# Performance work log

Measured on AMD Instinct MI355X. Metric: run time of the kernel, lower is better.

Reference implementation:

```python
import jax, jax.numpy as jnp
import numpy as np

OUT = 7  # output_size of AdaptiveMaxPool2d


def _roi_pool(images, rois, roi_idx):
    # images: [N,C,H,W]; rois: [R,4] rel coords (x1,y1,x2,y2); roi_idx: [R]
    n, c, h, w = images.shape
    x1 = jnp.floor(rois[:, 0] * w).astype(jnp.int32)
    y1 = jnp.floor(rois[:, 1] * h).astype(jnp.int32)
    x2 = jnp.ceil(rois[:, 2] * w).astype(jnp.int32)
    y2 = jnp.ceil(rois[:, 3] * h).astype(jnp.int32)
    Hr = y2 - y1  # per-ROI crop height
    Wr = x2 - x1  # per-ROI crop width

    feats = images[roi_idx]  # [R,C,H,W] gather per-ROI source image
    hh = jnp.arange(h)
    ww = jnp.arange(w)
    neg = jnp.finfo(images.dtype).min

    # Adaptive max pool is separable: max over row-bins, then col-bins.
    # PyTorch adaptive bins over a region of size L: [floor(i*L/OUT), ceil((i+1)*L/OUT))
    rows = []
    for i in range(OUT):  # small fixed loop over output rows
        s = y1 + (i * Hr) // OUT
        e = y1 + ((i + 1) * Hr + OUT - 1) // OUT  # ceil
        m = (hh[None, :] >= s[:, None]) & (hh[None, :] < e[:, None])  # [R,H]
        rows.append(jnp.max(jnp.where(m[:, None, :, None], feats, neg), axis=2))  # [R,C,W]
    rowp = jnp.stack(rows, axis=2)  # [R,C,OUT,W]

    cols = []
    for j in range(OUT):  # small fixed loop over output cols
        s = x1 + (j * Wr) // OUT
        e = x1 + ((j + 1) * Wr + OUT - 1) // OUT
        m = (ww[None, :] >= s[:, None]) & (ww[None, :] < e[:, None])  # [R,W]
        cols.append(jnp.max(jnp.where(m[:, None, None, :], rowp, neg), axis=3))  # [R,C,OUT]
    return jnp.stack(cols, axis=3)  # [R,C,OUT,OUT]


def setup_inputs() -> dict:
    key = jax.random.key(0)
    k1, k2, k3 = jax.random.split(key, 3)
    N, C, H, W, R = 8, 256, 56, 56, 256
    images = jax.random.normal(k1, (N, C, H, W), dtype=jnp.float32)
    # build valid boxes: x1<x2, y1<y2 in [0,1]
    pts = jax.random.uniform(k2, (R, 2, 2), dtype=jnp.float32)
    lo = jnp.min(pts, axis=1)
    hi = jnp.max(pts, axis=1)
    rois = jnp.stack([lo[:, 0], lo[:, 1], hi[:, 0], hi[:, 1]], axis=1)  # [R,4]
    roi_idx = jax.random.randint(k3, (R,), 0, N)
    return {"images": images, "rois": rois, "roi_idx": roi_idx}


def reference(images, rois, roi_idx):
    return _roi_pool(images, rois, roi_idx)
```

## Files before the change

### kernel.cpp

```cpp
#include <hip/hip_runtime.h>

#define OUTS 7
#define CC 256
#define HH 56
#define WW 56
#define PX (HH * WW)
#define STRIDE 58
#define SPLIT 2
#define MAXROI 96

typedef _Float16 half2_t __attribute__((ext_vector_type(2)));

__global__ __launch_bounds__(256) void roipool_kernel(
    const float* __restrict__ images, const float* __restrict__ rois,
    const int* __restrict__ roi_idx, float* __restrict__ out, int R)
{
    __shared__ __align__(16) uint2 plane[STRIDE * HH];
    __shared__ int    list[MAXROI];
    __shared__ unsigned short ys[MAXROI * 7];
    __shared__ unsigned short xs[MAXROI * 7];
    __shared__ int cnt;

    const int b  = blockIdx.x;
    const int s  = b & (SPLIT - 1);
    const int pq = b >> 1;
    const int n  = pq >> 6;
    const int c0 = (pq & 63) * 4;
    const int t  = threadIdx.x;

    if (t < 64) {
        int base = 0;
        #pragma unroll
        for (int k = 0; k < 4; ++k) {
            int r = k * 64 + t;
            bool match = (r < R) && (roi_idx[r] == n);
            unsigned long long mask = __ballot(match);
            int pos = base + __popcll(mask & ((1ULL << t) - 1ULL));
            if (match && pos < MAXROI) list[pos] = r;
            base += __popcll(mask);
        }
        if (t == 0) cnt = (base < MAXROI) ? base : MAXROI;
    }

    const float4* srcA = reinterpret_cast<const float4*>(images + (size_t)(n * CC + c0)     * PX);
    const float4* srcB = reinterpret_cast<const float4*>(images + (size_t)(n * CC + c0 + 1) * PX);
    const float4* srcC = reinterpret_cast<const float4*>(images + (size_t)(n * CC + c0 + 2) * PX);
    const float4* srcD = reinterpret_cast<const float4*>(images + (size_t)(n * CC + c0 + 3) * PX);
    #pragma unroll
    for (int k = 0; k < 4; ++k) {
        int idx = t + k * 256;
        if (idx < PX / 4) {
            float4 a = srcA[idx], bb = srcB[idx], cc = srcC[idx], dd = srcD[idx];
            const float* ap = &a.x; const float* bp = &bb.x;
            const float* cp = &cc.x; const float* dp = &dd.x;
            int y  = idx / 14;
            int x0 = (idx - y * 14) * 4;
            unsigned lo[4], hi[4];
            #pragma unroll
            for (int p = 0; p < 4; ++p) {
                half2_t l = { (_Float16)ap[p], (_Float16)bp[p] };
                half2_t h = { (_Float16)cp[p], (_Float16)dp[p] };
                lo[p] = __builtin_bit_cast(unsigned, l);
                hi[p] = __builtin_bit_cast(unsigned, h);
            }
            uint4* dst = reinterpret_cast<uint4*>(&plane[y * STRIDE + x0]);
            dst[0] = make_uint4(lo[0], hi[0], lo[1], hi[1]);
            dst[1] = make_uint4(lo[2], hi[2], lo[3], hi[3]);
        }
    }
    __syncthreads();

    const int count = cnt;

    for (int e = t; e < count * 7; e += 256) {
        int m = e / 7, i = e - m * 7;
        int r = list[m];
        float4 rv = reinterpret_cast<const float4*>(rois)[r];
        int x1 = (int)floorf(rv.x * (float)WW);
        int y1 = (int)floorf(rv.y * (float)HH);
        int x2 = (int)ceilf (rv.z * (float)WW);
        int y2 = (int)ceilf (rv.w * (float)HH);
        int Hr = y2 - y1, Wr = x2 - x1;
        int sy = y1 + (i * Hr) / 7, ey = y1 + ((i + 1) * Hr + 6) / 7;
        int sx = x1 + (i * Wr) / 7, ex = x1 + ((i + 1) * Wr + 6) / 7;
        ys[m * 7 + i] = (unsigned short)(sy | (ey << 8));
        xs[m * 7 + i] = (unsigned short)(sx | (ex << 8));
    }
    __syncthreads();

    const int wv   = t >> 6;
    const int lane = t & 63;
    const int i = lane / 7;
    const int j = lane - i * 7;

    if (lane < OUTS * OUTS) {
        const half2_t NEG = { (_Float16)-65504.0f, (_Float16)-65504.0f };
        for (int m = (wv << 1) + s; m < count; m += SPLIT * 4) {
            int r = list[m];
            int yse = ys[m * 7 + i];
            int xse = xs[m * 7 + j];
            int sy = yse & 255, ey = yse >> 8;
            int sx = xse & 255, ex = xse >> 8;

            half2_t a01 = NEG, a23 = NEG;

            for (int y = sy; y < ey; y += 2) {
                const uint2* r0 = plane + y * STRIDE;
                const uint2* r1 = plane + min(y + 1, ey - 1) * STRIDE;
                for (int x = sx; x < ex; x += 4) {
                    int xb = min(x + 1, ex - 1);
                    int xc = min(x + 2, ex - 1);
                    int xd = min(x + 3, ex - 1);
                    uint2 v0 = r0[x], v1 = r0[xb], v2 = r0[xc], v3 = r0[xd];
                    uint2 w0 = r1[x], w1 = r1[xb], w2 = r1[xc], w3 = r1[xd];
                    a01 = __builtin_elementwise_max(a01, __builtin_bit_cast(half2_t, v0.x));
                    a23 = __builtin_elementwise_max(a23, __builtin_bit_cast(half2_t, v0.y));
                    a01 = __builtin_elementwise_max(a01, __builtin_bit_cast(half2_t, v1.x));
                    a23 = __builtin_elementwise_max(a23, __builtin_bit_cast(half2_t, v1.y));
                    a01 = __builtin_elementwise_max(a01, __builtin_bit_cast(half2_t, v2.x));
                    a23 = __builtin_elementwise_max(a23, __builtin_bit_cast(half2_t, v2.y));
                    a01 = __builtin_elementwise_max(a01, __builtin_bit_cast(half2_t, v3.x));
                    a23 = __builtin_elementwise_max(a23, __builtin_bit_cast(half2_t, v3.y));
                    a01 = __builtin_elementwise_max(a01, __builtin_bit_cast(half2_t, w0.x));
                    a23 = __builtin_elementwise_max(a23, __builtin_bit_cast(half2_t, w0.y));
                    a01 = __builtin_elementwise_max(a01, __builtin_bit_cast(half2_t, w1.x));
                    a23 = __builtin_elementwise_max(a23, __builtin_bit_cast(half2_t, w1.y));
                    a01 = __builtin_elementwise_max(a01, __builtin_bit_cast(half2_t, w2.x));
                    a23 = __builtin_elementwise_max(a23, __builtin_bit_cast(half2_t, w2.y));
                    a01 = __builtin_elementwise_max(a01, __builtin_bit_cast(half2_t, w3.x));
                    a23 = __builtin_elementwise_max(a23, __builtin_bit_cast(half2_t, w3.y));
                }
            }

            bool ok = (ey > sy) && (ex > sx);
            const float NF = -3.402823466e+38f;
            float f0 = ok ? (float)a01.x : NF;
            float f1 = ok ? (float)a01.y : NF;
            float f2 = ok ? (float)a23.x : NF;
            float f3 = ok ? (float)a23.y : NF;

            size_t o = ((size_t)r * CC + c0) * (OUTS * OUTS) + lane;
            out[o]       = f0;
            out[o + 49]  = f1;
            out[o + 98]  = f2;
            out[o + 147] = f3;
        }
    }
}

extern "C" void kernel_launch(void* const* d_in, const int* in_sizes, int n_in,
                              void* d_out, int out_size, void* d_ws, size_t ws_size,
                              hipStream_t stream) {
    const float* images  = (const float*)d_in[0];
    const float* rois    = (const float*)d_in[1];
    const int*   roi_idx = (const int*)d_in[2];
    float* out = (float*)d_out;

    int R = in_sizes[2];
    int N = in_sizes[0] / (CC * PX);

    int grid = N * (CC / 4) * SPLIT;
    roipool_kernel<<<grid, 256, 0, stream>>>(images, rois, roi_idx, out, R);
}
```

Measured before the change: 87.60 us.

## Drop ROI split across blocks, precompute bins in wave 0, batch global loads

Removes the SPLIT=2 duplication, so each (image, 4-channel group) block loads its plane once and processes all of its ROIs, which halves global image traffic and the conversion work. Bin boundaries are now computed by the first wavefront right after list building, without a separate barrier. Image loads are issued all at once into registers before conversion, to get more memory-level parallelism. In exchange the grid has half as many blocks with twice the pooling work each, and register pressure rises.

```diff
diff --git a/kernel.cpp b/kernel.cpp
--- a/kernel.cpp
+++ b/kernel.cpp
@@ -6,7 +6,6 @@
 #define WW 56
 #define PX (HH * WW)
 #define STRIDE 58
-#define SPLIT 2
 #define MAXROI 96
 
 typedef _Float16 half2_t __attribute__((ext_vector_type(2)));
@@ -22,10 +21,8 @@
     __shared__ int cnt;
 
     const int b  = blockIdx.x;
-    const int s  = b & (SPLIT - 1);
-    const int pq = b >> 1;
-    const int n  = pq >> 6;
-    const int c0 = (pq & 63) * 4;
+    const int n  = b >> 6;
+    const int c0 = (b & 63) * 4;
     const int t  = threadIdx.x;
 
     if (t < 64) {
@@ -39,20 +36,43 @@
             if (match && pos < MAXROI) list[pos] = r;
             base += __popcll(mask);
         }
-        if (t == 0) cnt = (base < MAXROI) ? base : MAXROI;
+        int count0 = (base < MAXROI) ? base : MAXROI;
+        if (t == 0) cnt = count0;
+
+        for (int e = t; e < count0 * 7; e += 64) {
+            int m = e / 7, i = e - m * 7;
+            int r = list[m];
+            float4 rv = reinterpret_cast<const float4*>(rois)[r];
+            int x1 = (int)floorf(rv.x * (float)WW);
+            int y1 = (int)floorf(rv.y * (float)HH);
+            int x2 = (int)ceilf (rv.z * (float)WW);
+            int y2 = (int)ceilf (rv.w * (float)HH);
+            int Hr = y2 - y1, Wr = x2 - x1;
+            int sy = y1 + (i * Hr) / 7, ey = y1 + ((i + 1) * Hr + 6) / 7;
+            int sx = x1 + (i * Wr) / 7, ex = x1 + ((i + 1) * Wr + 6) / 7;
+            ys[m * 7 + i] = (unsigned short)(sy | (ey << 8));
+            xs[m * 7 + i] = (unsigned short)(sx | (ex << 8));
+        }
     }
 
-    const float4* srcA = reinterpret_cast<const float4*>(images + (size_t)(n * CC + c0)     * PX);
-    const float4* srcB = reinterpret_cast<const float4*>(images + (size_t)(n * CC + c0 + 1) * PX);
-    const float4* srcC = reinterpret_cast<const float4*>(images + (size_t)(n * CC + c0 + 2) * PX);
-    const float4* srcD = reinterpret_cast<const float4*>(images + (size_t)(n * CC + c0 + 3) * PX);
+    const float* base0 = images + (size_t)(n * CC + c0) * PX;
+    float4 ra[4], rb[4], rc[4], rd[4];
     #pragma unroll
     for (int k = 0; k < 4; ++k) {
         int idx = t + k * 256;
         if (idx < PX / 4) {
-            float4 a = srcA[idx], bb = srcB[idx], cc = srcC[idx], dd = srcD[idx];
-            const float* ap = &a.x; const float* bp = &bb.x;
-            const float* cp = &cc.x; const float* dp = &dd.x;
+            ra[k] = reinterpret_cast<const float4*>(base0)[idx];
+            rb[k] = reinterpret_cast<const float4*>(base0 + PX)[idx];
+            rc[k] = reinterpret_cast<const float4*>(base0 + 2 * PX)[idx];
+            rd[k] = reinterpret_cast<const float4*>(base0 + 3 * PX)[idx];
+        }
+    }
+    #pragma unroll
+    for (int k = 0; k < 4; ++k) {
+        int idx = t + k * 256;
+        if (idx < PX / 4) {
+            const float* ap = &ra[k].x; const float* bp = &rb[k].x;
+            const float* cp = &rc[k].x; const float* dp = &rd[k].x;
             int y  = idx / 14;
             int x0 = (idx - y * 14) * 4;
             unsigned lo[4], hi[4];
@@ -71,23 +91,6 @@
     __syncthreads();
 
     const int count = cnt;
-
-    for (int e = t; e < count * 7; e += 256) {
-        int m = e / 7, i = e - m * 7;
-        int r = list[m];
-        float4 rv = reinterpret_cast<const float4*>(rois)[r];
-        int x1 = (int)floorf(rv.x * (float)WW);
-        int y1 = (int)floorf(rv.y * (float)HH);
-        int x2 = (int)ceilf (rv.z * (float)WW);
-        int y2 = (int)ceilf (rv.w * (float)HH);
-        int Hr = y2 - y1, Wr = x2 - x1;
-        int sy = y1 + (i * Hr) / 7, ey = y1 + ((i + 1) * Hr + 6) / 7;
-        int sx = x1 + (i * Wr) / 7, ex = x1 + ((i + 1) * Wr + 6) / 7;
-        ys[m * 7 + i] = (unsigned short)(sy | (ey << 8));
-        xs[m * 7 + i] = (unsigned short)(sx | (ex << 8));
-    }
-    __syncthreads();
-
     const int wv   = t >> 6;
     const int lane = t & 63;
     const int i = lane / 7;
@@ -95,7 +98,7 @@
 
     if (lane < OUTS * OUTS) {
         const half2_t NEG = { (_Float16)-65504.0f, (_Float16)-65504.0f };
-        for (int m = (wv << 1) + s; m < count; m += SPLIT * 4) {
+        for (int m = wv; m < count; m += 4) {
             int r = list[m];
             int yse = ys[m * 7 + i];
             int xse = xs[m * 7 + j];
@@ -159,6 +162,6 @@
     int R = in_sizes[2];
     int N = in_sizes[0] / (CC * PX);
 
-    int grid = N * (CC / 4) * SPLIT;
+    int grid = N * (CC / 4);
     roipool_kernel<<<grid, 256, 0, stream>>>(images, rois, roi_idx, out, R);
 }
```

After: 88.09 us. No clear change (+0.5%).
